# Kernel optimization log

Measured on AMD Instinct MI355X. Metric: run time of the kernel, lower is better.

## Reference

```python
import jax, jax.numpy as jnp
import numpy as np

B, C, H, W = 8, 64, 256, 256  # H must equal W for the second matmul


def setup_inputs() -> dict:
    key = jax.random.key(0)
    kq, kk, kv = jax.random.split(key, 3)
    Q = jax.random.normal(kq, (B, C, H, W), dtype=jnp.float32)
    K = jax.random.normal(kk, (B, C, H, W), dtype=jnp.float32)
    V = jax.random.normal(kv, (B, C, H, W), dtype=jnp.float32)
    di = jnp.ones((1,), dtype=jnp.float32)  # learned scalar scale
    return {"Q": Q, "K": K, "V": V, "di": di}


def reference(Q, K, V, di):
    # similarity[b,c,i,k] = sum_w Q[b,c,i,w] * K[b,c,k,w], scaled by di
    sim = jnp.einsum('bciw,bckw->bcik', Q, K) * di[0]
    attn = jax.nn.softmax(sim, axis=-1)  # [B,C,H,H]
    # residual = attn @ V^T -> [B,C,H,H]; output is residual^T:
    # out[b,c,i,j] = sum_k attn[b,c,j,k] * V[b,c,i,k]
    out = jnp.einsum('bcjk,bcik->bcij', attn, V)
    return out
```

## Files before the change

kernel.cpp:

```cpp
#include <hip/hip_runtime.h>
#include <hip/hip_bf16.h>


typedef __attribute__((ext_vector_type(8))) _Float16 f16x8;
typedef __attribute__((ext_vector_type(4))) float f32x4;
typedef __attribute__((ext_vector_type(16))) float f32x16;

#define BARRIER() asm volatile("s_waitcnt lgkmcnt(0)\n\ts_barrier" ::: "memory")

__device__ __forceinline__ f32x4 mfma16h(f16x8 a, f16x8 b, f32x4 c) {
  return __builtin_amdgcn_mfma_f32_16x16x32_f16(a, b, c, 0, 0, 0);
}
__device__ __forceinline__ f32x16 mfma32h(f16x8 a, f16x8 b, f32x16 c) {
  return __builtin_amdgcn_mfma_f32_32x32x16_f16(a, b, c, 0, 0, 0);
}
__device__ __forceinline__ f16x8 cvt8(f32x4 a, f32x4 b) {
  f16x8 r;
  r[0] = (_Float16)a[0]; r[1] = (_Float16)a[1];
  r[2] = (_Float16)a[2]; r[3] = (_Float16)a[3];
  r[4] = (_Float16)b[0]; r[5] = (_Float16)b[1];
  r[6] = (_Float16)b[2]; r[7] = (_Float16)b[3];
  return r;
}
__device__ __forceinline__ int swzA(int row, int byteCol) {
  return row * 512 + (byteCol ^ ((row & 15) << 4));
}
__device__ __forceinline__ int swzV(int row, int byteCol) {
  return row * 256 + (byteCol ^ ((row & 15) << 4));
}

__global__ __launch_bounds__(512, 4) void attn_fused10(
    const float* __restrict__ Q, const float* __restrict__ K,
    const float* __restrict__ V, const float* __restrict__ di,
    float* __restrict__ out) {
  __shared__ short Kbuf[2][16 * 256];
  __shared__ short Abuf[128 * 256];
  short* Vlds = &Kbuf[0][0];

  const int t = threadIdx.x;
  const int lane = t & 63;
  const int wv = t >> 6;
  const int l15 = lane & 15;
  const int l4 = (lane >> 4) & 3;
  const int l31 = lane & 31;
  const int h5 = lane >> 5;

  const int bid = blockIdx.x;
  const int bc = (bid >> 4) * 8 + (bid & 7);
  const int j0 = ((bid >> 3) & 1) << 7;

  const float dival = di[0];
  const size_t base = (size_t)bc << 16;
  const float* Qs = Q + base;
  const float* Ks = K + base;
  const float* Vs = V + base;
  float* Os = out + base;

  const int sr = t >> 5;
  const int scb = (t & 31) << 4;

  f32x4 kpA0, kpA1, kpB0, kpB1;
  {
    const float* p = Ks + sr * 256 + (t & 31) * 8;
    kpA0 = *(const f32x4*)p;
    kpA1 = *(const f32x4*)(p + 4);
    const float* q = p + 4096;
    kpB0 = *(const f32x4*)q;
    kpB1 = *(const f32x4*)(q + 4);
  }
  f16x8 qh[8];
  {
    const float* qrow = Qs + (size_t)(j0 + 16 * wv + l15) * 256 + 8 * l4;
#pragma unroll
    for (int s = 0; s < 8; ++s)
      qh[s] = cvt8(*(const f32x4*)(qrow + 32 * s),
                   *(const f32x4*)(qrow + 32 * s + 4));
  }

  f32x4 acc[16];
#pragma unroll
  for (int i = 0; i < 16; ++i) acc[i] = (f32x4){0.f, 0.f, 0.f, 0.f};

#pragma unroll
  for (int ch = 0; ch < 16; ++ch) {
    short* kb = Kbuf[ch & 1];
    if ((ch & 1) == 0) {
      *(f16x8*)((char*)kb + swzA(sr, scb)) = cvt8(kpA0, kpA1);
      BARRIER();
      if (ch < 14) {
        const float* p = Ks + (ch + 2) * 4096 + sr * 256 + (t & 31) * 8;
        kpA0 = *(const f32x4*)p;
        kpA1 = *(const f32x4*)(p + 4);
      }
    } else {
      *(f16x8*)((char*)kb + swzA(sr, scb)) = cvt8(kpB0, kpB1);
      BARRIER();
      if (ch < 14) {
        const float* p = Ks + (ch + 2) * 4096 + sr * 256 + (t & 31) * 8;
        kpB0 = *(const f32x4*)p;
        kpB1 = *(const f32x4*)(p + 4);
      }
    }
    __builtin_amdgcn_s_setprio(1);
    f32x4 a = acc[ch];
#pragma unroll
    for (int s = 0; s < 8; ++s) {
      f16x8 bh = *(const f16x8*)((const char*)kb + swzA(l15, 64 * s + 16 * l4));
      a = mfma16h(qh[s], bh, a);
    }
    acc[ch] = a;
    __builtin_amdgcn_s_setprio(0);
  }

  const int vr = t >> 3;
  const int vcf = (t & 7) * 16;
  f32x4 vpA[4], vpB[4];
  {
    const float* p = Vs + (size_t)vr * 256 + vcf;
#pragma unroll
    for (int e = 0; e < 4; ++e) vpA[e] = *(const f32x4*)(p + 4 * e);
    const float* q = p + 128;
#pragma unroll
    for (int e = 0; e < 4; ++e) vpB[e] = *(const f32x4*)(q + 4 * e);
  }

  float mx[4] = {-1e30f, -1e30f, -1e30f, -1e30f};
#pragma unroll
  for (int idx = 0; idx < 16; ++idx)
#pragma unroll
    for (int r = 0; r < 4; ++r) {
      acc[idx][r] *= dival;
      mx[r] = fmaxf(mx[r], acc[idx][r]);
    }
#pragma unroll
  for (int o = 1; o <= 8; o <<= 1)
#pragma unroll
    for (int r = 0; r < 4; ++r) mx[r] = fmaxf(mx[r], __shfl_xor(mx[r], o));
  float sm[4] = {0.f, 0.f, 0.f, 0.f};
#pragma unroll
  for (int idx = 0; idx < 16; ++idx)
#pragma unroll
    for (int r = 0; r < 4; ++r) {
      acc[idx][r] = __expf(acc[idx][r] - mx[r]);
      sm[r] += acc[idx][r];
    }
#pragma unroll
  for (int o = 1; o <= 8; o <<= 1)
#pragma unroll
    for (int r = 0; r < 4; ++r) sm[r] += __shfl_xor(sm[r], o);
#pragma unroll
  for (int r = 0; r < 4; ++r) sm[r] = 1.0f / sm[r];
#pragma unroll
  for (int idx = 0; idx < 16; ++idx)
#pragma unroll
    for (int r = 0; r < 4; ++r) {
      const int row = 16 * wv + 4 * l4 + r;
      *(_Float16*)((char*)Abuf + swzA(row, 2 * (16 * idx + l15))) =
          (_Float16)(acc[idx][r] * sm[r]);
    }
  BARRIER();

  const int ig = wv >> 2;
  const int jg = wv & 3;
  f32x16 o = {};
#pragma unroll
  for (int cc = 0; cc < 8; ++cc) {
    const int kh = cc & 1;
    if ((cc & 1) == 0) {
      *(f16x8*)((char*)Vlds + swzV(vr, 2 * vcf)) = cvt8(vpA[0], vpA[1]);
      *(f16x8*)((char*)Vlds + swzV(vr, 2 * vcf + 16)) = cvt8(vpA[2], vpA[3]);
      BARRIER();
      if (cc < 6) {
        const float* p =
            Vs + (size_t)(64 * ((cc + 2) >> 1) + vr) * 256 + vcf;
#pragma unroll
        for (int e = 0; e < 4; ++e) vpA[e] = *(const f32x4*)(p + 4 * e);
      }
    } else {
      *(f16x8*)((char*)Vlds + swzV(vr, 2 * vcf)) = cvt8(vpB[0], vpB[1]);
      *(f16x8*)((char*)Vlds + swzV(vr, 2 * vcf + 16)) = cvt8(vpB[2], vpB[3]);
      BARRIER();
      if (cc < 6) {
        const float* p =
            Vs + (size_t)(64 * ((cc + 2) >> 1) + vr) * 256 + 128 + vcf;
#pragma unroll
        for (int e = 0; e < 4; ++e) vpB[e] = *(const f32x4*)(p + 4 * e);
      }
    }
    __builtin_amdgcn_s_setprio(1);
#pragma unroll
    for (int kk = 0; kk < 8; ++kk) {
      f16x8 vfrag = *(const f16x8*)((const char*)Vlds +
                                    swzV(32 * ig + l31, 32 * kk + 16 * h5));
      f16x8 pfrag =
          *(const f16x8*)((const char*)Abuf +
                          swzA(32 * jg + l31, 256 * kh + 32 * kk + 16 * h5));
      o = mfma32h(vfrag, pfrag, o);
    }
    __builtin_amdgcn_s_setprio(0);
    if (kh == 1) {
      const int rbase = 64 * (cc >> 1) + 32 * ig + 4 * h5;
      const int col = j0 + 32 * jg + l31;
#pragma unroll
      for (int reg = 0; reg < 16; ++reg) {
        const int rw = (reg & 3) + 8 * (reg >> 2);
        Os[(size_t)(rbase + rw) * 256 + col] = o[reg];
      }
      o = (f32x16){};
    }
    BARRIER();
  }
}

extern "C" void kernel_launch(void* const* d_in, const int* in_sizes, int n_in,
                              void* d_out, int out_size, void* d_ws,
                              size_t ws_size, hipStream_t stream) {
  const float* Q = (const float*)d_in[0];
  const float* K = (const float*)d_in[1];
  const float* V = (const float*)d_in[2];
  const float* di = (const float*)d_in[3];
  float* out = (float*)d_out;
  const int BC = in_sizes[0] / (256 * 256);
  hipLaunchKernelGGL(attn_fused10, dim3(BC * 2), dim3(512), 0, stream, Q, K, V,
                     di, out);
}
```

Baseline: 112.2 us.

## Process each (b,c) slice in one 1024-thread block sharing K/V staging

The two 512-thread blocks that each handled half the output columns of a (b,c) slice are merged into a single 1024-thread block covering all 256 rows. Each K and V chunk is now loaded from global memory and converted to fp16 once per slice instead of once per half. The per-thread staging loads shrink to match the larger block. The full 256x256 fp16 attention matrix in LDS grows to 128KB, which limits each CU to one resident block and reduces latency hiding between blocks.

```diff
diff --git a/kernel.cpp b/kernel.cpp
--- a/kernel.cpp
+++ b/kernel.cpp
@@ -29,12 +29,12 @@
   return row * 256 + (byteCol ^ ((row & 15) << 4));
 }
 
-__global__ __launch_bounds__(512, 4) void attn_fused10(
+__global__ __launch_bounds__(1024, 4) void attn_fused11(
     const float* __restrict__ Q, const float* __restrict__ K,
     const float* __restrict__ V, const float* __restrict__ di,
     float* __restrict__ out) {
   __shared__ short Kbuf[2][16 * 256];
-  __shared__ short Abuf[128 * 256];
+  __shared__ short Abuf[256 * 256];
   short* Vlds = &Kbuf[0][0];
 
   const int t = threadIdx.x;
@@ -45,9 +45,7 @@
   const int l31 = lane & 31;
   const int h5 = lane >> 5;
 
-  const int bid = blockIdx.x;
-  const int bc = (bid >> 4) * 8 + (bid & 7);
-  const int j0 = ((bid >> 3) & 1) << 7;
+  const int bc = blockIdx.x;
 
   const float dival = di[0];
   const size_t base = (size_t)bc << 16;
@@ -56,21 +54,18 @@
   const float* Vs = V + base;
   float* Os = out + base;
 
-  const int sr = t >> 5;
-  const int scb = (t & 31) << 4;
-
-  f32x4 kpA0, kpA1, kpB0, kpB1;
+  const int sr = t >> 6;
+  const int scf = (t & 63) << 2;
+
+  f32x4 kpA, kpB;
   {
-    const float* p = Ks + sr * 256 + (t & 31) * 8;
-    kpA0 = *(const f32x4*)p;
-    kpA1 = *(const f32x4*)(p + 4);
-    const float* q = p + 4096;
-    kpB0 = *(const f32x4*)q;
-    kpB1 = *(const f32x4*)(q + 4);
+    const float* p = Ks + sr * 256 + scf;
+    kpA = *(const f32x4*)p;
+    kpB = *(const f32x4*)(p + 4096);
   }
   f16x8 qh[8];
   {
-    const float* qrow = Qs + (size_t)(j0 + 16 * wv + l15) * 256 + 8 * l4;
+    const float* qrow = Qs + (size_t)(16 * wv + l15) * 256 + 8 * l4;
 #pragma unroll
     for (int s = 0; s < 8; ++s)
       qh[s] = cvt8(*(const f32x4*)(qrow + 32 * s),
@@ -84,22 +79,23 @@
 #pragma unroll
   for (int ch = 0; ch < 16; ++ch) {
     short* kb = Kbuf[ch & 1];
-    if ((ch & 1) == 0) {
-      *(f16x8*)((char*)kb + swzA(sr, scb)) = cvt8(kpA0, kpA1);
-      BARRIER();
-      if (ch < 14) {
-        const float* p = Ks + (ch + 2) * 4096 + sr * 256 + (t & 31) * 8;
-        kpA0 = *(const f32x4*)p;
-        kpA1 = *(const f32x4*)(p + 4);
-      }
-    } else {
-      *(f16x8*)((char*)kb + swzA(sr, scb)) = cvt8(kpB0, kpB1);
-      BARRIER();
-      if (ch < 14) {
-        const float* p = Ks + (ch + 2) * 4096 + sr * 256 + (t & 31) * 8;
-        kpB0 = *(const f32x4*)p;
-        kpB1 = *(const f32x4*)(p + 4);
-      }
+    {
+      _Float16 h4[4];
+      f32x4 src = ((ch & 1) == 0) ? kpA : kpB;
+      h4[0] = (_Float16)src[0];
+      h4[1] = (_Float16)src[1];
+      h4[2] = (_Float16)src[2];
+      h4[3] = (_Float16)src[3];
+      *(unsigned long long*)((char*)kb + swzA(sr, scf * 2)) =
+          *(unsigned long long*)h4;
+    }
+    BARRIER();
+    if (ch < 14) {
+      const float* p = Ks + (ch + 2) * 4096 + sr * 256 + scf;
+      if ((ch & 1) == 0)
+        kpA = *(const f32x4*)p;
+      else
+        kpB = *(const f32x4*)p;
     }
     __builtin_amdgcn_s_setprio(1);
     f32x4 a = acc[ch];
@@ -112,16 +108,16 @@
     __builtin_amdgcn_s_setprio(0);
   }
 
-  const int vr = t >> 3;
-  const int vcf = (t & 7) * 16;
-  f32x4 vpA[4], vpB[4];
+  const int vr = t >> 4;
+  const int vcf = (t & 15) * 8;
+  f32x4 vpA[2], vpB[2];
   {
     const float* p = Vs + (size_t)vr * 256 + vcf;
-#pragma unroll
-    for (int e = 0; e < 4; ++e) vpA[e] = *(const f32x4*)(p + 4 * e);
+    vpA[0] = *(const f32x4*)p;
+    vpA[1] = *(const f32x4*)(p + 4);
     const float* q = p + 128;
-#pragma unroll
-    for (int e = 0; e < 4; ++e) vpB[e] = *(const f32x4*)(q + 4 * e);
+    vpB[0] = *(const f32x4*)q;
+    vpB[1] = *(const f32x4*)(q + 4);
   }
 
   float mx[4] = {-1e30f, -1e30f, -1e30f, -1e30f};
@@ -160,31 +156,28 @@
     }
   BARRIER();
 
-  const int ig = wv >> 2;
-  const int jg = wv & 3;
+  const int ig = wv & 1;
+  const int jg = wv >> 1;
   f32x16 o = {};
 #pragma unroll
   for (int cc = 0; cc < 8; ++cc) {
     const int kh = cc & 1;
     if ((cc & 1) == 0) {
       *(f16x8*)((char*)Vlds + swzV(vr, 2 * vcf)) = cvt8(vpA[0], vpA[1]);
-      *(f16x8*)((char*)Vlds + swzV(vr, 2 * vcf + 16)) = cvt8(vpA[2], vpA[3]);
       BARRIER();
       if (cc < 6) {
-        const float* p =
-            Vs + (size_t)(64 * ((cc + 2) >> 1) + vr) * 256 + vcf;
-#pragma unroll
-        for (int e = 0; e < 4; ++e) vpA[e] = *(const f32x4*)(p + 4 * e);
+        const float* p = Vs + (size_t)(64 * ((cc + 2) >> 1) + vr) * 256 + vcf;
+        vpA[0] = *(const f32x4*)p;
+        vpA[1] = *(const f32x4*)(p + 4);
       }
     } else {
       *(f16x8*)((char*)Vlds + swzV(vr, 2 * vcf)) = cvt8(vpB[0], vpB[1]);
-      *(f16x8*)((char*)Vlds + swzV(vr, 2 * vcf + 16)) = cvt8(vpB[2], vpB[3]);
       BARRIER();
       if (cc < 6) {
         const float* p =
             Vs + (size_t)(64 * ((cc + 2) >> 1) + vr) * 256 + 128 + vcf;
-#pragma unroll
-        for (int e = 0; e < 4; ++e) vpB[e] = *(const f32x4*)(p + 4 * e);
+        vpB[0] = *(const f32x4*)p;
+        vpB[1] = *(const f32x4*)(p + 4);
       }
     }
     __builtin_amdgcn_s_setprio(1);
@@ -200,7 +193,7 @@
     __builtin_amdgcn_s_setprio(0);
     if (kh == 1) {
       const int rbase = 64 * (cc >> 1) + 32 * ig + 4 * h5;
-      const int col = j0 + 32 * jg + l31;
+      const int col = 32 * jg + l31;
 #pragma unroll
       for (int reg = 0; reg < 16; ++reg) {
         const int rw = (reg & 3) + 8 * (reg >> 2);
@@ -221,6 +214,6 @@
   const float* di = (const float*)d_in[3];
   float* out = (float*)d_out;
   const int BC = in_sizes[0] / (256 * 256);
-  hipLaunchKernelGGL(attn_fused10, dim3(BC * 2), dim3(512), 0, stream, Q, K, V,
+  hipLaunchKernelGGL(attn_fused11, dim3(BC), dim3(1024), 0, stream, Q, K, V,
                      di, out);
 }
```

New measurement: 106.8 us. 1.05x faster.
